# Kernel optimization log

Measured on AMD Instinct MI355X. Metric: run time of the kernel, lower is better.

## Reference

```python
import jax, jax.numpy as jnp
import numpy as np

ALPHA = 0.2  # LeakyReLU negative slope
NEG_INF = -9e15

def setup_inputs() -> dict:
    key = jax.random.key(0)
    k1, k2, k3, k4, k5 = jax.random.split(key, 5)
    B, N, Fin, Fout = 8, 2048, 128, 128
    h = jax.random.normal(k1, (B, N, Fin), dtype=jnp.float32)
    adj = jax.random.randint(k2, (N, N), 0, 2, dtype=jnp.int32)
    dist = jax.random.uniform(k3, (N, N), dtype=jnp.float32)
    W = jax.random.normal(k4, (Fin, Fout), dtype=jnp.float32) * (1.414 * (6.0 / (Fin + Fout)) ** 0.5)
    a = jax.random.normal(k5, (2 * Fout, 1), dtype=jnp.float32) * 0.1
    distance_scaler = jnp.ones((1,), dtype=jnp.float32)
    return {"h": h, "adj": adj, "dist": dist, "W": W, "a": a, "distance_scaler": distance_scaler}

def reference(h, adj, dist, W, a, distance_scaler):
    # h: [B,N,Fin], adj/dist: [N,N], W: [Fin,Fout], a: [2*Fout,1]
    h_prime = jnp.einsum('bnf,fh->bnh', h, W)              # [B,N,Fout]
    Fout = h_prime.shape[-1]
    a1, a2 = a[:Fout, 0], a[Fout:, 0]
    # additive score: a1.h_i + a2.h_j, equivalent to cat([h_i,h_j]) @ a
    si = h_prime @ a1                                      # [B,N]
    sj = h_prime @ a2                                      # [B,N]
    e = jax.nn.leaky_relu(si[:, :, None] + sj[:, None, :], negative_slope=ALPHA)  # [B,N,N]
    dist_bias = -jnp.log(dist + 1e-6) * distance_scaler[0]  # [N,N]
    scores = e + dist_bias[None, :, :]
    scores = jnp.where(adj[None, :, :] > 0, scores, NEG_INF)
    attention = jax.nn.softmax(scores, axis=2)             # [B,N,N]
    # dropout=identity in eval mode
    out = jnp.einsum('bij,bjh->bih', attention, h_prime)   # [B,N,Fout]
    return jax.nn.elu(out)
```

## Files before the change

### kernel.cpp

```cpp
#include <hip/hip_runtime.h>
#include <hip/hip_bf16.h>

typedef __attribute__((ext_vector_type(4))) float f32x4;
typedef __attribute__((ext_vector_type(8))) short short8;
typedef __attribute__((ext_vector_type(4))) unsigned short ushort4v;
typedef _Float16 f16x8 __attribute__((ext_vector_type(8)));

#define NB 8
#define NN 2048
#define NF 128
#define LOG2E 1.4426950408889634f
#define MASK_NEG_H -60000.0f

static __device__ __forceinline__ unsigned short f2bf(float f) {
    union { __hip_bfloat16 b; unsigned short u; } cv;
    cv.b = __float2bfloat16(f);
    return cv.u;
}

__global__ __launch_bounds__(256) void k_pre(
    const float* __restrict__ h, const int* __restrict__ adj,
    const float* __restrict__ dist, const float* __restrict__ W,
    const float* __restrict__ a, const float* __restrict__ scaler,
    unsigned short* __restrict__ vfrag, float* __restrict__ siC,
    float* __restrict__ sjC, _Float16* __restrict__ biasF)
{
    __shared__ __align__(16) unsigned char smem[34816];
    const int bid = blockIdx.x;
    const int t = threadIdx.x;

    if (bid < 256) {
        unsigned char* WT = smem;
        float* wa1 = (float*)(smem + 32768);
        float* wa2 = wa1 + NF;

        const int lane = t & 63;
        const int w = t >> 6;
        const int b = bid >> 5;
        const int i0 = (bid & 31) << 6;

        {
            const int f = t >> 1;
            const int c0 = (t & 1) << 6;
            float s1 = 0.f, s2 = 0.f;
            const float* wrow = W + f * NF + c0;
            const float* a1p = a + c0;
            const float* a2p = a + NF + c0;
            #pragma unroll 8
            for (int c = 0; c < 64; ++c) {
                float wv = wrow[c];
                s1 += wv * a1p[c];
                s2 += wv * a2p[c];
                int col = c0 + c;
                int dst = col * 256 + ((2 * f) ^ ((col & 15) << 4));
                *reinterpret_cast<unsigned short*>(&WT[dst]) = f2bf(wv);
            }
            s1 += __shfl_xor(s1, 1);
            s2 += __shfl_xor(s2, 1);
            if ((t & 1) == 0) { wa1[f] = s1 * LOG2E; wa2[f] = s2 * LOG2E; }
        }
        __syncthreads();

        const int l15 = lane & 15;
        const int arow = i0 + w * 16 + l15;
        const int kofs = (lane >> 4) << 3;
        const float* hrow = h + (size_t)(b * NN + arow) * NF + kofs;
        const int swz = l15 << 4;

        f32x4 acc[8];
        #pragma unroll
        for (int nt = 0; nt < 8; ++nt) acc[nt] = (f32x4)(0.f);
        float s1 = 0.f, s2 = 0.f;

        #pragma unroll
        for (int k0 = 0; k0 < NF; k0 += 32) {
            f32x4 h0 = *reinterpret_cast<const f32x4*>(hrow + k0);
            f32x4 h1 = *reinterpret_cast<const f32x4*>(hrow + k0 + 4);
            f32x4 w1lo = *reinterpret_cast<const f32x4*>(&wa1[k0 + kofs]);
            f32x4 w1hi = *reinterpret_cast<const f32x4*>(&wa1[k0 + kofs + 4]);
            f32x4 w2lo = *reinterpret_cast<const f32x4*>(&wa2[k0 + kofs]);
            f32x4 w2hi = *reinterpret_cast<const f32x4*>(&wa2[k0 + kofs + 4]);
            short8 af;
            #pragma unroll
            for (int e = 0; e < 4; ++e) {
                s1 += h0[e] * w1lo[e] + h1[e] * w1hi[e];
                s2 += h0[e] * w2lo[e] + h1[e] * w2hi[e];
                af[e]     = (short)f2bf(h0[e]);
                af[4 + e] = (short)f2bf(h1[e]);
            }
            const int ib = (2 * (k0 + kofs)) ^ swz;
            #pragma unroll
            for (int nt = 0; nt < 8; ++nt) {
                short8 bf8 = *reinterpret_cast<short8*>(&WT[(nt * 16 + l15) * 256 + ib]);
                acc[nt] = __builtin_amdgcn_mfma_f32_16x16x32_bf16(af, bf8, acc[nt], 0, 0, 0);
            }
        }

        s1 += __shfl_xor(s1, 16); s1 += __shfl_xor(s1, 32);
        s2 += __shfl_xor(s2, 16); s2 += __shfl_xor(s2, 32);
        if (lane < 16) {
            siC[b * NN + arow] = s1;
            sjC[b * NN + arow] = s2;
        }

        const int J0 = i0 + w * 16 + ((lane >> 4) << 2);
        const int s = J0 >> 5;
        const int jq = (J0 >> 3) & 3;
        const int eh = J0 & 7;
        #pragma unroll
        for (int nt = 0; nt < 8; ++nt) {
            ushort4v pk;
            #pragma unroll
            for (int e = 0; e < 4; ++e) pk[e] = f2bf(acc[nt][e]);
            *reinterpret_cast<ushort4v*>(
                vfrag + (((size_t)(b * 64 + s) * 8 + nt) * 64 + (l15 | (jq << 4))) * 8 + eh) = pk;
        }
    } else {
        _Float16 (*st)[64][8] = (_Float16 (*)[64][8])smem;
        const int bid2 = bid - 256;
        const int iblk = bid2 >> 3;
        const int jch = bid2 & 7;
        const int i_l = t >> 4;
        const int o2 = t & 15;
        const int i = iblk * 16 + i_l;
        const int jbase = jch * 256 + o2 * 16;
        const float sc = scaler[0];

        const int* ap = adj + (size_t)i * NN + jbase;
        const float* dp = dist + (size_t)i * NN + jbase;
        int av[16]; float dv[16];
        *reinterpret_cast<int4*>(&av[0])  = *reinterpret_cast<const int4*>(ap);
        *reinterpret_cast<int4*>(&av[4])  = *reinterpret_cast<const int4*>(ap + 4);
        *reinterpret_cast<int4*>(&av[8])  = *reinterpret_cast<const int4*>(ap + 8);
        *reinterpret_cast<int4*>(&av[12]) = *reinterpret_cast<const int4*>(ap + 12);
        *reinterpret_cast<float4*>(&dv[0])  = *reinterpret_cast<const float4*>(dp);
        *reinterpret_cast<float4*>(&dv[4])  = *reinterpret_cast<const float4*>(dp + 4);
        *reinterpret_cast<float4*>(&dv[8])  = *reinterpret_cast<const float4*>(dp + 8);
        *reinterpret_cast<float4*>(&dv[12]) = *reinterpret_cast<const float4*>(dp + 12);

        #pragma unroll
        for (int u = 0; u < 2; ++u) {
            const int sl = (o2 * 2 + u) >> 2;
            const int jq = (o2 * 2 + u) & 3;
            f16x8 pk;
            #pragma unroll
            for (int e = 0; e < 8; ++e) {
                const int idx = u * 8 + e;
                float v = (av[idx] > 0) ? (-__log2f(dv[idx] + 1e-6f) * sc) : MASK_NEG_H;
                pk[e] = (_Float16)v;
            }
            *reinterpret_cast<f16x8*>(&st[sl][i_l | (jq << 4)][0]) = pk;
        }
        __syncthreads();

        const int w = t >> 6, lane = t & 63;
        #pragma unroll
        for (int sub = 0; sub < 2; ++sub) {
            const int fs = w * 2 + sub;
            *reinterpret_cast<f16x8*>(
                biasF + ((size_t)(iblk * 64 + jch * 8 + fs) * 64 + lane) * 8) =
                *reinterpret_cast<f16x8*>(&st[fs][lane][0]);
        }
    }
}

__global__ __launch_bounds__(512, 8) void k_attn(
    const unsigned short* __restrict__ vfrag, const float* __restrict__ siC,
    const float* __restrict__ sjC, const _Float16* __restrict__ biasF,
    float* __restrict__ out)
{
    __shared__ __align__(16) float red[4][1024];
    __shared__ float lp[4][2][16];

    const int t = threadIdx.x;
    const int lane = t & 63;
    const int w = t >> 6;
    const int rw = w & 1;
    const int jq = w >> 1;
    const int l15 = lane & 15;
    const int hi = lane >> 4;

    const int bid = blockIdx.x;
    const int xcd = bid & 7;
    const int seq = bid >> 3;
    const int rg = (xcd & 3) * 16 + (seq >> 3);
    const int b  = (xcd >> 2) * 4 + ((seq >> 1) & 3);
    const int ch = seq & 1;

    const int rowbase = rg * 32 + rw * 16;
    const float si0 = siC[b * NN + rowbase + l15];

    const float* sjp = sjC + b * NN + jq * 512 + hi * 8;
    const int iblk = rg * 2 + rw;
    const _Float16* bp = biasF + ((size_t)(iblk * 64 + jq * 16) * 64 + lane) * 8;
    const unsigned short* vpp = vfrag +
        (((size_t)(b * 64 + jq * 16) * 8) + ch * 4) * 512 + lane * 8;

    f32x4 acc[4];
    #pragma unroll
    for (int ct = 0; ct < 4; ++ct) acc[ct] = (f32x4)(0.f);
    float ls0 = 0.f;

    #pragma unroll 4
    for (int sl = 0; sl < 16; ++sl) {
        f32x4 sj0 = *reinterpret_cast<const f32x4*>(sjp + sl * 32);
        f32x4 sj1 = *reinterpret_cast<const f32x4*>(sjp + sl * 32 + 4);
        f16x8 bv = *reinterpret_cast<const f16x8*>(bp + sl * 512);
        short8 pa;
        #pragma unroll
        for (int e = 0; e < 8; ++e) {
            const float sjv = (e < 4) ? sj0[e] : sj1[e - 4];
            float x = si0 + sjv;
            x = fmaxf(x, 0.2f * x) + (float)bv[e];
            float p = __builtin_amdgcn_exp2f(x);
            ls0 += p;
            pa[e] = (short)f2bf(p);
        }
        const unsigned short* vs = vpp + sl * 4096;
        #pragma unroll
        for (int ct = 0; ct < 4; ++ct) {
            const short8 bfr = *reinterpret_cast<const short8*>(vs + ct * 512);
            acc[ct] = __builtin_amdgcn_mfma_f32_16x16x32_bf16(pa, bfr, acc[ct], 0, 0, 0);
        }
    }

    ls0 += __shfl_xor(ls0, 16);
    ls0 += __shfl_xor(ls0, 32);
    if (lane < 16) lp[jq][rw][l15] = ls0;

    #define WACC(buf) { _Pragma("unroll") for (int ct = 0; ct < 4; ++ct)       \
        *reinterpret_cast<f32x4*>(&red[buf][(ct * 64 + lane) * 4]) = acc[ct]; }
    #define AACC(buf) { _Pragma("unroll") for (int ct = 0; ct < 4; ++ct)       \
        acc[ct] += *reinterpret_cast<const f32x4*>(                            \
            &red[buf][(ct * 64 + lane) * 4]); }

    if (jq == 1) WACC(rw * 2)
    if (jq == 3) WACC(rw * 2 + 1)
    __syncthreads();
    if (jq == 0) AACC(rw * 2)
    if (jq == 2) AACC(rw * 2 + 1)
    __syncthreads();
    if (jq == 2) WACC(rw * 2)
    __syncthreads();
    if (jq == 0) {
        AACC(rw * 2)
        float linv[4];
        #pragma unroll
        for (int e = 0; e < 4; ++e) {
            const int rr = (hi << 2) + e;
            linv[e] = 1.0f / (lp[0][rw][rr] + lp[1][rw][rr]
                            + lp[2][rw][rr] + lp[3][rw][rr]);
        }
        #pragma unroll
        for (int ct = 0; ct < 4; ++ct) {
            const int col = ch * 64 + ct * 16 + l15;
            #pragma unroll
            for (int e = 0; e < 4; ++e) {
                const int row = rowbase + (hi << 2) + e;
                float v = acc[ct][e] * linv[e];
                v = (v > 0.f) ? v : expm1f(v);
                out[(size_t)(b * NN + row) * NF + col] = v;
            }
        }
    }
    #undef WACC
    #undef AACC
}

extern "C" void kernel_launch(void* const* d_in, const int* in_sizes, int n_in,
                              void* d_out, int out_size, void* d_ws, size_t ws_size,
                              hipStream_t stream) {
    (void)in_sizes; (void)n_in; (void)out_size; (void)ws_size;
    const float* h      = (const float*)d_in[0];
    const int*   adj    = (const int*)d_in[1];
    const float* dist   = (const float*)d_in[2];
    const float* W      = (const float*)d_in[3];
    const float* a      = (const float*)d_in[4];
    const float* scaler = (const float*)d_in[5];
    float* out = (float*)d_out;

    char* ws = (char*)d_ws;
    unsigned short* vfrag = (unsigned short*)ws;
    float* siC      = (float*)(ws + 4 * 1024 * 1024);
    float* sjC      = (float*)(ws + 4 * 1024 * 1024 + 65536);
    _Float16* biasF = (_Float16*)(ws + 4 * 1024 * 1024 + 2 * 65536);

    k_pre<<<dim3(1280), dim3(256), 0, stream>>>(h, adj, dist, W, a, scaler,
                                                vfrag, siC, sjC, biasF);
    k_attn<<<dim3(NB * NN / 16), dim3(512), 0, stream>>>(vfrag, siC, sjC, biasF, out);
}
```

Before: 50.47 us.

## Restructure attention blocks to cover full feature width with two-way key split

Each attention block now handles 64 rows and all 128 output features, splitting the key dimension in two instead of four. This removes the duplicated score/exp computation across the two feature halves and shortens the cross-wave reduction to a single shared-memory exchange. The trade-off is fewer, larger blocks (one per CU), more accumulator registers, and a relaxed occupancy hint, which may reduce latency hiding.

```diff
diff --git a/kernel.cpp b/kernel.cpp
--- a/kernel.cpp
+++ b/kernel.cpp
@@ -164,45 +164,41 @@
     }
 }
 
-__global__ __launch_bounds__(512, 8) void k_attn(
+__global__ __launch_bounds__(512, 4) void k_attn(
     const unsigned short* __restrict__ vfrag, const float* __restrict__ siC,
     const float* __restrict__ sjC, const _Float16* __restrict__ biasF,
     float* __restrict__ out)
 {
-    __shared__ __align__(16) float red[4][1024];
-    __shared__ float lp[4][2][16];
+    __shared__ __align__(16) float red[4][8][64][4];
+    __shared__ float lp[2][4][16];
 
     const int t = threadIdx.x;
     const int lane = t & 63;
     const int w = t >> 6;
-    const int rw = w & 1;
-    const int jq = w >> 1;
+    const int rt = w & 3;
+    const int jh = w >> 2;
     const int l15 = lane & 15;
     const int hi = lane >> 4;
 
-    const int bid = blockIdx.x;
-    const int xcd = bid & 7;
-    const int seq = bid >> 3;
-    const int rg = (xcd & 3) * 16 + (seq >> 3);
-    const int b  = (xcd >> 2) * 4 + ((seq >> 1) & 3);
-    const int ch = seq & 1;
-
-    const int rowbase = rg * 32 + rw * 16;
+    const int b = blockIdx.x & 7;
+    const int rg = blockIdx.x >> 3;
+
+    const int rowbase = rg * 64 + rt * 16;
     const float si0 = siC[b * NN + rowbase + l15];
 
-    const float* sjp = sjC + b * NN + jq * 512 + hi * 8;
-    const int iblk = rg * 2 + rw;
-    const _Float16* bp = biasF + ((size_t)(iblk * 64 + jq * 16) * 64 + lane) * 8;
-    const unsigned short* vpp = vfrag +
-        (((size_t)(b * 64 + jq * 16) * 8) + ch * 4) * 512 + lane * 8;
-
-    f32x4 acc[4];
+    const float* sjp = sjC + b * NN + jh * 1024 + hi * 8;
+    const _Float16* bp = biasF +
+        ((size_t)((rg * 4 + rt) * 64 + jh * 32) * 64 + lane) * 8;
+    const unsigned short* vp = vfrag +
+        ((size_t)(b * 64 + jh * 32) * 8) * 512 + lane * 8;
+
+    f32x4 acc[8];
     #pragma unroll
-    for (int ct = 0; ct < 4; ++ct) acc[ct] = (f32x4)(0.f);
+    for (int ct = 0; ct < 8; ++ct) acc[ct] = (f32x4)(0.f);
     float ls0 = 0.f;
 
-    #pragma unroll 4
-    for (int sl = 0; sl < 16; ++sl) {
+    #pragma unroll 2
+    for (int sl = 0; sl < 32; ++sl) {
         f32x4 sj0 = *reinterpret_cast<const f32x4*>(sjp + sl * 32);
         f32x4 sj1 = *reinterpret_cast<const f32x4*>(sjp + sl * 32 + 4);
         f16x8 bv = *reinterpret_cast<const f16x8*>(bp + sl * 512);
@@ -216,9 +212,9 @@
             ls0 += p;
             pa[e] = (short)f2bf(p);
         }
-        const unsigned short* vs = vpp + sl * 4096;
-        #pragma unroll
-        for (int ct = 0; ct < 4; ++ct) {
+        const unsigned short* vs = vp + sl * 4096;
+        #pragma unroll
+        for (int ct = 0; ct < 8; ++ct) {
             const short8 bfr = *reinterpret_cast<const short8*>(vs + ct * 512);
             acc[ct] = __builtin_amdgcn_mfma_f32_16x16x32_bf16(pa, bfr, acc[ct], 0, 0, 0);
         }
@@ -226,45 +222,34 @@
 
     ls0 += __shfl_xor(ls0, 16);
     ls0 += __shfl_xor(ls0, 32);
-    if (lane < 16) lp[jq][rw][l15] = ls0;
-
-    #define WACC(buf) { _Pragma("unroll") for (int ct = 0; ct < 4; ++ct)       \
-        *reinterpret_cast<f32x4*>(&red[buf][(ct * 64 + lane) * 4]) = acc[ct]; }
-    #define AACC(buf) { _Pragma("unroll") for (int ct = 0; ct < 4; ++ct)       \
-        acc[ct] += *reinterpret_cast<const f32x4*>(                            \
-            &red[buf][(ct * 64 + lane) * 4]); }
-
-    if (jq == 1) WACC(rw * 2)
-    if (jq == 3) WACC(rw * 2 + 1)
+    if (lane < 16) lp[jh][rt][l15] = ls0;
+
+    if (jh == 1) {
+        #pragma unroll
+        for (int ct = 0; ct < 8; ++ct)
+            *reinterpret_cast<f32x4*>(&red[rt][ct][lane][0]) = acc[ct];
+    }
     __syncthreads();
-    if (jq == 0) AACC(rw * 2)
-    if (jq == 2) AACC(rw * 2 + 1)
-    __syncthreads();
-    if (jq == 2) WACC(rw * 2)
-    __syncthreads();
-    if (jq == 0) {
-        AACC(rw * 2)
+    if (jh == 0) {
         float linv[4];
         #pragma unroll
         for (int e = 0; e < 4; ++e) {
             const int rr = (hi << 2) + e;
-            linv[e] = 1.0f / (lp[0][rw][rr] + lp[1][rw][rr]
-                            + lp[2][rw][rr] + lp[3][rw][rr]);
-        }
-        #pragma unroll
-        for (int ct = 0; ct < 4; ++ct) {
-            const int col = ch * 64 + ct * 16 + l15;
+            linv[e] = 1.0f / (lp[0][rt][rr] + lp[1][rt][rr]);
+        }
+        #pragma unroll
+        for (int ct = 0; ct < 8; ++ct) {
+            f32x4 o = acc[ct] + *reinterpret_cast<const f32x4*>(&red[rt][ct][lane][0]);
+            const int col = ct * 16 + l15;
             #pragma unroll
             for (int e = 0; e < 4; ++e) {
                 const int row = rowbase + (hi << 2) + e;
-                float v = acc[ct][e] * linv[e];
+                float v = o[e] * linv[e];
                 v = (v > 0.f) ? v : expm1f(v);
                 out[(size_t)(b * NN + row) * NF + col] = v;
             }
         }
     }
-    #undef WACC
-    #undef AACC
 }
 
 extern "C" void kernel_launch(void* const* d_in, const int* in_sizes, int n_in,
@@ -287,5 +272,5 @@
 
     k_pre<<<dim3(1280), dim3(256), 0, stream>>>(h, adj, dist, W, a, scaler,
                                                 vfrag, siC, sjC, biasF);
-    k_attn<<<dim3(NB * NN / 16), dim3(512), 0, stream>>>(vfrag, siC, sjC, biasF, out);
-}
+    k_attn<<<dim3(NB * NN / 64), dim3(512), 0, stream>>>(vfrag, siC, sjC, biasF, out);
+}
```

New measurement: 46.76 us. 7.3% less time.
